# Kernel optimization log

Measured on AMD Instinct MI355X. Metric: run time of the kernel, lower is better.

Reference implementation:

```python
import jax, jax.numpy as jnp
import numpy as np

HEADS = 4
DIM_HEAD = 32
SCALE = DIM_HEAD ** -0.5


def setup_inputs() -> dict:
    key = jax.random.key(0)
    k1, k2, k3 = jax.random.split(key, 3)
    dim = 256
    hidden = HEADS * DIM_HEAD  # 128
    x = jax.random.normal(k1, (2, dim, 64, 64), dtype=jnp.float32)
    # Conv2d 1x1 weights flattened to [out_ch, in_ch]
    w_qkv = jax.random.normal(k2, (hidden * 3, dim), dtype=jnp.float32) * (dim ** -0.5)
    w_out = jax.random.normal(k3, (dim, hidden), dtype=jnp.float32) * (hidden ** -0.5)
    b_out = jnp.zeros((dim,), dtype=jnp.float32)
    return {"x": x, "w_qkv": w_qkv, "w_out": w_out, "b_out": b_out}


def reference(x, w_qkv, w_out, b_out):
    b, c, h, w = x.shape
    n = h * w
    # 1x1 conv == channel matmul: [b, 3*hidden, h, w]
    qkv = jnp.einsum('bchw,oc->bohw', x, w_qkv)
    q, k, v = jnp.split(qkv, 3, axis=1)
    # 'b (heads d) x y -> b heads d (x y)'
    def to_heads(t):
        return t.reshape(b, HEADS, DIM_HEAD, n)
    q, k, v = to_heads(q), to_heads(k), to_heads(v)
    q = q * SCALE
    dots = jnp.einsum('bhdi,bhdj->bhij', q, k)  # [b, heads, n, n]
    dots = dots - jax.lax.stop_gradient(jnp.max(dots, axis=-1, keepdims=True))
    attn = jax.nn.softmax(dots, axis=-1)
    out = jnp.einsum('bhij,bhdj->bhid', attn, v)  # [b, heads, n, d]
    # 'b heads (x y) d -> b (heads d) x y'
    out = out.transpose(0, 1, 3, 2).reshape(b, HEADS * DIM_HEAD, h, w)
    return jnp.einsum('bchw,oc->bohw', out, w_out) + b_out[None, :, None, None]
```

## Files before the change

kernel.cpp:

```cpp
#include <hip/hip_runtime.h>
#include <hip/hip_bf16.h>
#include <math.h>

#define NB 2
#define CIN 256
#define NPOS 4096
#define HID 128
#define NHEAD 4
#define DHEAD 32
#define NBH 8
#define NSPLIT 4
#define QSCALE 0.2550348676144781f

typedef __bf16 bf16;
typedef __attribute__((ext_vector_type(8))) __bf16 bf16x8;
typedef __attribute__((ext_vector_type(4))) __bf16 bf16x4;
typedef __attribute__((ext_vector_type(4))) float f32x4;

union B8 { bf16x8 v; bf16x4 h[2]; };

#define XT_OFF  0u
#define QB_OFF  4194304u
#define KB_OFF  6291456u
#define VT_OFF  8388608u
#define AOP_OFF 10485760u
#define LP_OFF  18874368u
#define WB_OFF  19398656u
#define WOB_OFF 19595264u

__global__ __launch_bounds__(256) void prep_kernel(const float* __restrict__ x,
                                                   const float* __restrict__ wqkv,
                                                   const float* __restrict__ wout,
                                                   bf16* __restrict__ xt,
                                                   bf16* __restrict__ wb,
                                                   bf16* __restrict__ wob) {
    const int t = threadIdx.x;
    if (blockIdx.y == 4) {
        int tid = blockIdx.x * 256 + t;
        if (blockIdx.z == 0) {
            #pragma unroll
            for (int u = 0; u < 6; ++u) {
                int idx = tid * 6 + u;
                float v = wqkv[idx];
                if (idx < 32768) v *= QSCALE;
                wb[idx] = (bf16)v;
            }
        } else {
            wob[tid * 2]     = (bf16)wout[tid * 2];
            wob[tid * 2 + 1] = (bf16)wout[tid * 2 + 1];
        }
        return;
    }
    const int b  = blockIdx.z;
    const int c0 = blockIdx.y * 64;
    const int i0 = blockIdx.x * 64;
    __shared__ float Ts[64][65];
    const float* xb = x + (size_t)b * CIN * NPOS;
    #pragma unroll
    for (int u = 0; u < 4; ++u) {
        int c = (t >> 4) + u * 16;
        int i = (t & 15) * 4;
        float4 v = *(const float4*)(xb + (size_t)(c0 + c) * NPOS + i0 + i);
        Ts[c][i] = v.x; Ts[c][i + 1] = v.y; Ts[c][i + 2] = v.z; Ts[c][i + 3] = v.w;
    }
    __syncthreads();
    int i  = t & 63;
    int cc = (t >> 6) * 16;
    B8 o0, o1;
    #pragma unroll
    for (int j = 0; j < 8; ++j) {
        o0.v[j] = (bf16)Ts[cc + j][i];
        o1.v[j] = (bf16)Ts[cc + 8 + j][i];
    }
    bf16* dst = xt + ((size_t)b * NPOS + i0 + i) * CIN + c0 + cc;
    *(bf16x8*)dst       = o0.v;
    *(bf16x8*)(dst + 8) = o1.v;
}

__global__ __launch_bounds__(256) void qkv_kernel(const bf16* __restrict__ xt,
                                                  const bf16* __restrict__ wb,
                                                  bf16* __restrict__ qb,
                                                  bf16* __restrict__ kb,
                                                  bf16* __restrict__ vtb) {
    const int i0 = blockIdx.x * 64;
    const int ot = blockIdx.y * 64;
    const int b  = blockIdx.z;
    const int t  = threadIdx.x;
    const int w  = t >> 6;
    const int lane = t & 63;
    const int quad = lane >> 4;
    const int li   = lane & 15;

    __shared__ bf16 Bs[64][36];

    f32x4 acc[4];
    #pragma unroll
    for (int n = 0; n < 4; ++n) acc[n] = (f32x4){0.f, 0.f, 0.f, 0.f};

    const bf16* xrow = xt + ((size_t)b * NPOS + i0) * CIN;
    const int si = t >> 2;
    const int sk = (t & 3) * 8;

    for (int k0 = 0; k0 < CIN; k0 += 32) {
        __syncthreads();
        B8 g0;
        g0.v = *(const bf16x8*)(xrow + (size_t)si * CIN + k0 + sk);
        *(bf16x4*)&Bs[si][sk]     = g0.h[0];
        *(bf16x4*)&Bs[si][sk + 4] = g0.h[1];
        __syncthreads();
        bf16x8 afrag = *(const bf16x8*)(wb + (size_t)(ot + w * 16 + li) * CIN + k0 + quad * 8);
        #pragma unroll
        for (int n = 0; n < 4; ++n) {
            B8 bf;
            bf.h[0] = *(const bf16x4*)&Bs[n * 16 + li][quad * 8];
            bf.h[1] = *(const bf16x4*)&Bs[n * 16 + li][quad * 8 + 4];
            acc[n] = __builtin_amdgcn_mfma_f32_16x16x32_bf16(afrag, bf.v, acc[n], 0, 0, 0);
        }
    }

    const int obase = ot + w * 16;
    const int sect  = obase >> 7;
    const int oo    = obase & 127;
    const int h     = oo >> 5;
    const int dbase = (oo & 31) + quad * 4;
    const int bh    = b * NHEAD + h;

    #pragma unroll
    for (int n = 0; n < 4; ++n) {
        int i = i0 + n * 16 + li;
        f32x4 v = acc[n];
        if (sect <= 1) {
            bf16x4 pk;
            #pragma unroll
            for (int r = 0; r < 4; ++r) pk[r] = (bf16)v[r];
            bf16* base = (sect == 0) ? qb : kb;
            *(bf16x4*)(base + ((size_t)bh * NPOS + i) * DHEAD + dbase) = pk;
        } else {
            const int ip = i0 + ((n >> 1) << 5) + ((li >> 2) << 3) + ((n & 1) << 2) + (li & 3);
            #pragma unroll
            for (int r = 0; r < 4; ++r)
                vtb[((size_t)bh * DHEAD + dbase + r) * NPOS + ip] = (bf16)v[r];
        }
    }
}

__global__ __launch_bounds__(256, 4) void fattn_kernel(const bf16* __restrict__ qb,
                                                       const bf16* __restrict__ kb,
                                                       const bf16* __restrict__ vtb,
                                                       bf16* __restrict__ aop,
                                                       float* __restrict__ lpart) {
    const int id    = blockIdx.x;
    const int g     = id & 31;
    const int iblk  = id >> 5;
    const int bh    = g >> 2;
    const int split = g & 3;
    const int w     = threadIdx.x >> 6;
    const int lane  = threadIdx.x & 63;
    const int quad  = lane >> 4;
    const int li    = lane & 15;
    const int i0    = iblk * 128 + w * 32;
    const int j_lo  = split * 1024;

    const bf16* qrow = qb + (size_t)bh * NPOS * DHEAD;
    const bf16x8 qf0 = *(const bf16x8*)(qrow + (size_t)(i0 + li) * DHEAD + quad * 8);
    const bf16x8 qf1 = *(const bf16x8*)(qrow + (size_t)(i0 + 16 + li) * DHEAD + quad * 8);
    const bf16* kbase  = kb  + (size_t)bh * NPOS * DHEAD;
    const bf16* vtbase = vtb + (size_t)bh * DHEAD * NPOS;

    bf16x8 ones;
    #pragma unroll
    for (int j = 0; j < 8; ++j) ones[j] = (bf16)1.0f;

    f32x4 o00 = {0.f,0.f,0.f,0.f}, o01 = {0.f,0.f,0.f,0.f};
    f32x4 o10 = {0.f,0.f,0.f,0.f}, o11 = {0.f,0.f,0.f,0.f};
    f32x4 l0  = {0.f,0.f,0.f,0.f}, l1  = {0.f,0.f,0.f,0.f};

    __shared__ alignas(16) bf16 Kbuf[2][64][32];
    __shared__ alignas(16) bf16 Vbuf[2][32][64];

    const f32x4 zero = {0.f,0.f,0.f,0.f};

    const int krow = w * 16 + (lane >> 2);
    const int kcol = (lane & 3) * 8;
    const int vrow = w * 8 + (lane >> 3);
    const int vchk = lane & 7;
    const int vslot = vchk ^ (vrow & 7);
    const bf16* ksrc = kbase + (size_t)krow * DHEAD + kcol;
    const bf16* vsrc = vtbase + (size_t)vrow * NPOS + vchk * 8;

    bf16x8 kg, vg;

    kg = *(const bf16x8*)(ksrc + (size_t)j_lo * DHEAD);
    vg = *(const bf16x8*)(vsrc + j_lo);
    *(bf16x8*)&Kbuf[0][krow][kcol]      = kg;
    *(bf16x8*)&Vbuf[0][vrow][vslot * 8] = vg;
    __syncthreads();

    for (int it = 0; it < 16; ++it) {
        const int cur = it & 1;
        const int j0  = j_lo + it * 64;
        if (it < 15) {
            kg = *(const bf16x8*)(ksrc + (size_t)(j0 + 64) * DHEAD);
            vg = *(const bf16x8*)(vsrc + j0 + 64);
        }
        bf16x8 kf[4];
        #pragma unroll
        for (int tt = 0; tt < 4; ++tt)
            kf[tt] = *(const bf16x8*)&Kbuf[cur][16 * tt + li][quad * 8];
        f32x4 s0[4], s1[4];
        #pragma unroll
        for (int tt = 0; tt < 4; ++tt) {
            s0[tt] = __builtin_amdgcn_mfma_f32_16x16x32_bf16(kf[tt], qf0, zero, 0, 0, 0);
            s1[tt] = __builtin_amdgcn_mfma_f32_16x16x32_bf16(kf[tt], qf1, zero, 0, 0, 0);
        }
        #pragma unroll
        for (int h2 = 0; h2 < 2; ++h2) {
            B8 pa0, pa1;
            #pragma unroll
            for (int r = 0; r < 4; ++r) {
                pa0.v[r]     = (bf16)__builtin_amdgcn_exp2f(s0[2 * h2][r]);
                pa0.v[4 + r] = (bf16)__builtin_amdgcn_exp2f(s0[2 * h2 + 1][r]);
                pa1.v[r]     = (bf16)__builtin_amdgcn_exp2f(s1[2 * h2][r]);
                pa1.v[4 + r] = (bf16)__builtin_amdgcn_exp2f(s1[2 * h2 + 1][r]);
            }
            const int s0s = (h2 * 4 + quad) ^ (li & 7);
            bf16x8 v0f = *(const bf16x8*)&Vbuf[cur][li][s0s * 8];
            bf16x8 v1f = *(const bf16x8*)&Vbuf[cur][16 + li][s0s * 8];
            l0  = __builtin_amdgcn_mfma_f32_16x16x32_bf16(ones, pa0.v, l0,  0, 0, 0);
            l1  = __builtin_amdgcn_mfma_f32_16x16x32_bf16(ones, pa1.v, l1,  0, 0, 0);
            o00 = __builtin_amdgcn_mfma_f32_16x16x32_bf16(v0f,  pa0.v, o00, 0, 0, 0);
            o01 = __builtin_amdgcn_mfma_f32_16x16x32_bf16(v1f,  pa0.v, o01, 0, 0, 0);
            o10 = __builtin_amdgcn_mfma_f32_16x16x32_bf16(v0f,  pa1.v, o10, 0, 0, 0);
            o11 = __builtin_amdgcn_mfma_f32_16x16x32_bf16(v1f,  pa1.v, o11, 0, 0, 0);
        }
        if (it < 15) {
            *(bf16x8*)&Kbuf[cur ^ 1][krow][kcol]      = kg;
            *(bf16x8*)&Vbuf[cur ^ 1][vrow][vslot * 8] = vg;
        }
        __syncthreads();
    }

    const int b = bh >> 2, h = bh & 3;
    {
        const int i = i0 + li;
        bf16* dst = aop + (((size_t)(split * NB + b) * NPOS + i) * HID) + h * DHEAD;
        bf16x4 pk0, pk1;
        #pragma unroll
        for (int r = 0; r < 4; ++r) { pk0[r] = (bf16)o00[r]; pk1[r] = (bf16)o01[r]; }
        *(bf16x4*)(dst + quad * 4)      = pk0;
        *(bf16x4*)(dst + 16 + quad * 4) = pk1;
        if (quad == 0) lpart[((size_t)split * NBH + bh) * NPOS + i] = l0[0];
    }
    {
        const int i = i0 + 16 + li;
        bf16* dst = aop + (((size_t)(split * NB + b) * NPOS + i) * HID) + h * DHEAD;
        bf16x4 pk0, pk1;
        #pragma unroll
        for (int r = 0; r < 4; ++r) { pk0[r] = (bf16)o10[r]; pk1[r] = (bf16)o11[r]; }
        *(bf16x4*)(dst + quad * 4)      = pk0;
        *(bf16x4*)(dst + 16 + quad * 4) = pk1;
        if (quad == 0) lpart[((size_t)split * NBH + bh) * NPOS + i] = l1[0];
    }
}

__global__ __launch_bounds__(256) void proj_kernel(const bf16* __restrict__ aop,
                                                   const float* __restrict__ lpart,
                                                   const bf16* __restrict__ wob,
                                                   const float* __restrict__ bout,
                                                   float* __restrict__ y) {
    const int i0 = blockIdx.x * 16;
    const int b  = blockIdx.y;
    const int t  = threadIdx.x;
    const int w  = t >> 6;
    const int lane = t & 63;
    const int quad = lane >> 4;
    const int li   = lane & 15;

    __shared__ bf16 Bs[16][132];

    {
        const int row = t >> 4;
        const int cp  = (t & 15) * 8;
        const int gi  = i0 + row;
        const int h   = cp >> 5;

        float lsum = 0.f;
        #pragma unroll
        for (int s = 0; s < NSPLIT; ++s)
            lsum += lpart[((size_t)s * NBH + b * NHEAD + h) * NPOS + gi];
        const float invl = __builtin_amdgcn_rcpf(lsum);

        float vals[8];
        #pragma unroll
        for (int j = 0; j < 8; ++j) vals[j] = 0.f;
        #pragma unroll
        for (int s = 0; s < NSPLIT; ++s) {
            bf16x8 u = *(const bf16x8*)(aop + (((size_t)(s * NB + b) * NPOS + gi) * HID) + cp);
            #pragma unroll
            for (int j = 0; j < 8; ++j) vals[j] += (float)u[j];
        }
        B8 pk;
        #pragma unroll
        for (int j = 0; j < 8; ++j) pk.v[j] = (bf16)(vals[j] * invl);
        *(bf16x4*)&Bs[row][cp]     = pk.h[0];
        *(bf16x4*)&Bs[row][cp + 4] = pk.h[1];
    }
    __syncthreads();

    f32x4 acc[4];
    #pragma unroll
    for (int m = 0; m < 4; ++m) acc[m] = (f32x4){0.f, 0.f, 0.f, 0.f};

    #pragma unroll
    for (int k0 = 0; k0 < HID; k0 += 32) {
        B8 bf;
        bf.h[0] = *(const bf16x4*)&Bs[li][k0 + quad * 8];
        bf.h[1] = *(const bf16x4*)&Bs[li][k0 + quad * 8 + 4];
        #pragma unroll
        for (int m = 0; m < 4; ++m) {
            bf16x8 afrag = *(const bf16x8*)(wob + (size_t)(w * 64 + m * 16 + li) * HID + k0 + quad * 8);
            acc[m] = __builtin_amdgcn_mfma_f32_16x16x32_bf16(afrag, bf.v, acc[m], 0, 0, 0);
        }
    }

    float* yb = y + (size_t)b * CIN * NPOS;
    #pragma unroll
    for (int m = 0; m < 4; ++m) {
        const int oc = w * 64 + m * 16 + quad * 4;
        #pragma unroll
        for (int r = 0; r < 4; ++r)
            yb[(size_t)(oc + r) * NPOS + i0 + li] = acc[m][r] + bout[oc + r];
    }
}

extern "C" void kernel_launch(void* const* d_in, const int* in_sizes, int n_in,
                              void* d_out, int out_size, void* d_ws, size_t ws_size,
                              hipStream_t stream) {
    const float* x    = (const float*)d_in[0];
    const float* wqkv = (const float*)d_in[1];
    const float* wout = (const float*)d_in[2];
    const float* bout = (const float*)d_in[3];
    float* y = (float*)d_out;
    char* ws = (char*)d_ws;

    bf16*  xt  = (bf16*)(ws + XT_OFF);
    bf16*  qb  = (bf16*)(ws + QB_OFF);
    bf16*  kb  = (bf16*)(ws + KB_OFF);
    bf16*  vtb = (bf16*)(ws + VT_OFF);
    bf16*  aop = (bf16*)(ws + AOP_OFF);
    float* lp  = (float*)(ws + LP_OFF);
    bf16*  wb  = (bf16*)(ws + WB_OFF);
    bf16*  wob = (bf16*)(ws + WOB_OFF);

    prep_kernel<<<dim3(64, 5, 2), 256, 0, stream>>>(x, wqkv, wout, xt, wb, wob);
    qkv_kernel<<<dim3(64, 6, 2), 256, 0, stream>>>(xt, wb, qb, kb, vtb);
    fattn_kernel<<<dim3(1024), 256, 0, stream>>>(qb, kb, vtb, aop, lp);
    proj_kernel<<<dim3(256, 2), 256, 0, stream>>>(aop, lp, wob, bout, y);
}
```

Baseline: 102.9 us.

## Fuse input transpose and weight conversion into the QKV projection kernel

```diff
diff --git a/kernel.cpp b/kernel.cpp
--- a/kernel.cpp
+++ b/kernel.cpp
@@ -19,127 +19,100 @@
 
 union B8 { bf16x8 v; bf16x4 h[2]; };
 
-#define XT_OFF  0u
-#define QB_OFF  4194304u
-#define KB_OFF  6291456u
-#define VT_OFF  8388608u
-#define AOP_OFF 10485760u
-#define LP_OFF  18874368u
-#define WB_OFF  19398656u
-#define WOB_OFF 19595264u
-
-__global__ __launch_bounds__(256) void prep_kernel(const float* __restrict__ x,
-                                                   const float* __restrict__ wqkv,
-                                                   const float* __restrict__ wout,
-                                                   bf16* __restrict__ xt,
-                                                   bf16* __restrict__ wb,
-                                                   bf16* __restrict__ wob) {
-    const int t = threadIdx.x;
-    if (blockIdx.y == 4) {
-        int tid = blockIdx.x * 256 + t;
-        if (blockIdx.z == 0) {
-            #pragma unroll
-            for (int u = 0; u < 6; ++u) {
-                int idx = tid * 6 + u;
-                float v = wqkv[idx];
-                if (idx < 32768) v *= QSCALE;
-                wb[idx] = (bf16)v;
-            }
-        } else {
-            wob[tid * 2]     = (bf16)wout[tid * 2];
-            wob[tid * 2 + 1] = (bf16)wout[tid * 2 + 1];
-        }
-        return;
-    }
-    const int b  = blockIdx.z;
-    const int c0 = blockIdx.y * 64;
-    const int i0 = blockIdx.x * 64;
-    __shared__ float Ts[64][65];
-    const float* xb = x + (size_t)b * CIN * NPOS;
-    #pragma unroll
-    for (int u = 0; u < 4; ++u) {
-        int c = (t >> 4) + u * 16;
-        int i = (t & 15) * 4;
-        float4 v = *(const float4*)(xb + (size_t)(c0 + c) * NPOS + i0 + i);
-        Ts[c][i] = v.x; Ts[c][i + 1] = v.y; Ts[c][i + 2] = v.z; Ts[c][i + 3] = v.w;
-    }
-    __syncthreads();
-    int i  = t & 63;
-    int cc = (t >> 6) * 16;
-    B8 o0, o1;
-    #pragma unroll
-    for (int j = 0; j < 8; ++j) {
-        o0.v[j] = (bf16)Ts[cc + j][i];
-        o1.v[j] = (bf16)Ts[cc + 8 + j][i];
-    }
-    bf16* dst = xt + ((size_t)b * NPOS + i0 + i) * CIN + c0 + cc;
-    *(bf16x8*)dst       = o0.v;
-    *(bf16x8*)(dst + 8) = o1.v;
-}
-
-__global__ __launch_bounds__(256) void qkv_kernel(const bf16* __restrict__ xt,
-                                                  const bf16* __restrict__ wb,
+#define QB_OFF  0u
+#define KB_OFF  2097152u
+#define VT_OFF  4194304u
+#define LP_OFF  6291456u
+#define AOP_OFF 6815744u
+
+__global__ __launch_bounds__(512) void qkv_kernel(const float* __restrict__ x,
+                                                  const float* __restrict__ wqkv,
                                                   bf16* __restrict__ qb,
                                                   bf16* __restrict__ kb,
                                                   bf16* __restrict__ vtb) {
-    const int i0 = blockIdx.x * 64;
-    const int ot = blockIdx.y * 64;
-    const int b  = blockIdx.z;
+    const int i0 = blockIdx.x * 32;
+    const int b  = blockIdx.y;
     const int t  = threadIdx.x;
     const int w  = t >> 6;
     const int lane = t & 63;
     const int quad = lane >> 4;
     const int li   = lane & 15;
 
-    __shared__ bf16 Bs[64][36];
-
-    f32x4 acc[4];
-    #pragma unroll
-    for (int n = 0; n < 4; ++n) acc[n] = (f32x4){0.f, 0.f, 0.f, 0.f};
-
-    const bf16* xrow = xt + ((size_t)b * NPOS + i0) * CIN;
-    const int si = t >> 2;
-    const int sk = (t & 3) * 8;
-
+    __shared__ bf16 Bs[32][260];
+
+    {
+        const int il = (t & 7) * 4;
+        #pragma unroll
+        for (int u = 0; u < 4; ++u) {
+            const int c = (t >> 3) + u * 64;
+            float4 v = *(const float4*)(x + ((size_t)b * CIN + c) * NPOS + i0 + il);
+            Bs[il    ][c] = (bf16)v.x;
+            Bs[il + 1][c] = (bf16)v.y;
+            Bs[il + 2][c] = (bf16)v.z;
+            Bs[il + 3][c] = (bf16)v.w;
+        }
+    }
+    __syncthreads();
+
+    f32x4 acc[2][3];
+    #pragma unroll
+    for (int n = 0; n < 2; ++n)
+        #pragma unroll
+        for (int m = 0; m < 3; ++m) acc[n][m] = (f32x4){0.f,0.f,0.f,0.f};
+
+    #pragma unroll
     for (int k0 = 0; k0 < CIN; k0 += 32) {
-        __syncthreads();
-        B8 g0;
-        g0.v = *(const bf16x8*)(xrow + (size_t)si * CIN + k0 + sk);
-        *(bf16x4*)&Bs[si][sk]     = g0.h[0];
-        *(bf16x4*)&Bs[si][sk + 4] = g0.h[1];
-        __syncthreads();
-        bf16x8 afrag = *(const bf16x8*)(wb + (size_t)(ot + w * 16 + li) * CIN + k0 + quad * 8);
-        #pragma unroll
-        for (int n = 0; n < 4; ++n) {
-            B8 bf;
-            bf.h[0] = *(const bf16x4*)&Bs[n * 16 + li][quad * 8];
-            bf.h[1] = *(const bf16x4*)&Bs[n * 16 + li][quad * 8 + 4];
-            acc[n] = __builtin_amdgcn_mfma_f32_16x16x32_bf16(afrag, bf.v, acc[n], 0, 0, 0);
-        }
-    }
-
-    const int obase = ot + w * 16;
-    const int sect  = obase >> 7;
-    const int oo    = obase & 127;
-    const int h     = oo >> 5;
-    const int dbase = (oo & 31) + quad * 4;
-    const int bh    = b * NHEAD + h;
-
-    #pragma unroll
-    for (int n = 0; n < 4; ++n) {
-        int i = i0 + n * 16 + li;
-        f32x4 v = acc[n];
-        if (sect <= 1) {
-            bf16x4 pk;
-            #pragma unroll
-            for (int r = 0; r < 4; ++r) pk[r] = (bf16)v[r];
-            bf16* base = (sect == 0) ? qb : kb;
-            *(bf16x4*)(base + ((size_t)bh * NPOS + i) * DHEAD + dbase) = pk;
-        } else {
-            const int ip = i0 + ((n >> 1) << 5) + ((li >> 2) << 3) + ((n & 1) << 2) + (li & 3);
-            #pragma unroll
-            for (int r = 0; r < 4; ++r)
-                vtb[((size_t)bh * DHEAD + dbase + r) * NPOS + ip] = (bf16)v[r];
+        B8 bfr[2];
+        #pragma unroll
+        for (int n = 0; n < 2; ++n) {
+            bfr[n].h[0] = *(const bf16x4*)&Bs[n * 16 + li][k0 + quad * 8];
+            bfr[n].h[1] = *(const bf16x4*)&Bs[n * 16 + li][k0 + quad * 8 + 4];
+        }
+        #pragma unroll
+        for (int m = 0; m < 3; ++m) {
+            const int orow = w * 48 + m * 16 + li;
+            const float* wa = wqkv + (size_t)orow * CIN + k0 + quad * 8;
+            float4 a0 = *(const float4*)wa;
+            float4 a1 = *(const float4*)(wa + 4);
+            B8 af;
+            #pragma unroll
+            for (int j = 0; j < 4; ++j) { af.v[j] = (bf16)(&a0.x)[j]; af.v[4 + j] = (bf16)(&a1.x)[j]; }
+            #pragma unroll
+            for (int n = 0; n < 2; ++n)
+                acc[n][m] = __builtin_amdgcn_mfma_f32_16x16x32_bf16(af.v, bfr[n].v, acc[n][m], 0, 0, 0);
+        }
+    }
+
+    #pragma unroll
+    for (int m = 0; m < 3; ++m) {
+        const int obase = w * 48 + m * 16;
+        const int sect  = obase >> 7;
+        const int oo    = obase & 127;
+        const int h     = oo >> 5;
+        const int dbase = (oo & 31) + quad * 4;
+        const int bh    = b * NHEAD + h;
+        #pragma unroll
+        for (int n = 0; n < 2; ++n) {
+            int i = i0 + n * 16 + li;
+            f32x4 v = acc[n][m];
+            if (sect == 0) {
+                #pragma unroll
+                for (int r = 0; r < 4; ++r) v[r] *= QSCALE;
+            }
+            if (sect <= 1) {
+                bf16x4 pk;
+                #pragma unroll
+                for (int r = 0; r < 4; ++r) pk[r] = (bf16)v[r];
+                bf16* base = (sect == 0) ? qb : kb;
+                *(bf16x4*)(base + ((size_t)bh * NPOS + i) * DHEAD + dbase) = pk;
+            } else {
+                const int ng = ((i0 >> 4) & 2) | n;
+                const int ip = (i0 & ~63) + ((ng >> 1) << 5) + ((li >> 2) << 3)
+                             + ((ng & 1) << 2) + (li & 3);
+                #pragma unroll
+                for (int r = 0; r < 4; ++r)
+                    vtb[((size_t)bh * DHEAD + dbase + r) * NPOS + ip] = (bf16)v[r];
+            }
         }
     }
 }
@@ -265,7 +238,7 @@
 
 __global__ __launch_bounds__(256) void proj_kernel(const bf16* __restrict__ aop,
                                                    const float* __restrict__ lpart,
-                                                   const bf16* __restrict__ wob,
+                                                   const float* __restrict__ wout,
                                                    const float* __restrict__ bout,
                                                    float* __restrict__ y) {
     const int i0 = blockIdx.x * 16;
@@ -318,8 +291,13 @@
         bf.h[1] = *(const bf16x4*)&Bs[li][k0 + quad * 8 + 4];
         #pragma unroll
         for (int m = 0; m < 4; ++m) {
-            bf16x8 afrag = *(const bf16x8*)(wob + (size_t)(w * 64 + m * 16 + li) * HID + k0 + quad * 8);
-            acc[m] = __builtin_amdgcn_mfma_f32_16x16x32_bf16(afrag, bf.v, acc[m], 0, 0, 0);
+            const float* wa = wout + (size_t)(w * 64 + m * 16 + li) * HID + k0 + quad * 8;
+            float4 a0 = *(const float4*)wa;
+            float4 a1 = *(const float4*)(wa + 4);
+            B8 af;
+            #pragma unroll
+            for (int j = 0; j < 4; ++j) { af.v[j] = (bf16)(&a0.x)[j]; af.v[4 + j] = (bf16)(&a1.x)[j]; }
+            acc[m] = __builtin_amdgcn_mfma_f32_16x16x32_bf16(af.v, bf.v, acc[m], 0, 0, 0);
         }
     }
 
@@ -343,17 +321,13 @@
     float* y = (float*)d_out;
     char* ws = (char*)d_ws;
 
-    bf16*  xt  = (bf16*)(ws + XT_OFF);
     bf16*  qb  = (bf16*)(ws + QB_OFF);
     bf16*  kb  = (bf16*)(ws + KB_OFF);
     bf16*  vtb = (bf16*)(ws + VT_OFF);
+    float* lp  = (float*)(ws + LP_OFF);
     bf16*  aop = (bf16*)(ws + AOP_OFF);
-    float* lp  = (float*)(ws + LP_OFF);
-    bf16*  wb  = (bf16*)(ws + WB_OFF);
-    bf16*  wob = (bf16*)(ws + WOB_OFF);
-
-    prep_kernel<<<dim3(64, 5, 2), 256, 0, stream>>>(x, wqkv, wout, xt, wb, wob);
-    qkv_kernel<<<dim3(64, 6, 2), 256, 0, stream>>>(xt, wb, qb, kb, vtb);
+
+    qkv_kernel<<<dim3(128, 2), 512, 0, stream>>>(x, wqkv, qb, kb, vtb);
     fattn_kernel<<<dim3(1024), 256, 0, stream>>>(qb, kb, vtb, aop, lp);
-    proj_kernel<<<dim3(256, 2), 256, 0, stream>>>(aop, lp, wob, bout, y);
+    proj_kernel<<<dim3(256, 2), 256, 0, stream>>>(aop, lp, wout, bout, y);
 }
```

New measurement: 112.0 us. 1.09x slower.
